# Kernel tuning notes

Hardware: AMD Instinct MI355X
Metric: run time of the kernel (lower is better)

Reference implementation:

```python
import jax, jax.numpy as jnp
import numpy as np

H = 4096   # hidden_size
B = 8      # batch_size
N = 200    # total_nodes (<=200 so the undocumented sampler branch is not taken)
E = 400    # total_edges
TOPK_STARTS = 3   # min(3, nodes_in_batch)
# With max_hops=min(4,2)=2 and max_paths=min(8,4)=4, BFS yields only length-2
# paths and each start contributes paths[:4//3]=1 path: its first valid edge.


def _lin_init(k, fan_in, shape):
    s = 1.0 / np.sqrt(fan_in)
    return jax.random.uniform(k, shape, jnp.float32, -s, s)


def setup_inputs() -> dict:
    key = jax.random.key(0)
    ks = jax.random.split(key, 12)
    return {
        "query": jax.random.normal(ks[0], (B, H), jnp.float32),
        "node_features": jax.random.normal(ks[1], (N, H), jnp.float32),
        "Wq": _lin_init(ks[2], H, (H, H)), "bq": _lin_init(ks[3], H, (H,)),
        "Wn": _lin_init(ks[4], H, (H, H)), "bn": _lin_init(ks[5], H, (H,)),
        "W1": _lin_init(ks[6], H, (H, H)), "b1": _lin_init(ks[7], H, (H,)),
        "W2": _lin_init(ks[8], H, (H, H)), "b2": _lin_init(ks[9], H, (H,)),
        "ln_g": jnp.ones((H,), jnp.float32), "ln_b": jnp.zeros((H,), jnp.float32),
        "edge_index": jax.random.randint(ks[10], (2, E), 0, N),
        "batch_indices": jnp.sort(jax.random.randint(ks[11], (N,), 0, B)),
    }


def reference(query, node_features, Wq, bq, Wn, bn, W1, b1, W2, b2, ln_g, ln_b,
              edge_index, batch_indices):
    qp = query @ Wq.T + bq              # [B,H] query_projection
    npj = node_features @ Wn.T + bn     # [N,H] node_projection

    # cosine similarity (torch F.cosine_similarity, eps=1e-8), masked per batch
    qn = jnp.linalg.norm(qp, axis=-1, keepdims=True)   # [B,1]
    nn_ = jnp.linalg.norm(npj, axis=-1)                # [N]
    sim = (qp @ npj.T) / jnp.maximum(qn * nn_[None, :], 1e-8)   # [B,N]
    node_mask = batch_indices[None, :] == jnp.arange(B)[:, None]  # [B,N]
    sim_m = jnp.where(node_mask, sim, -jnp.inf)
    _, starts = jax.lax.top_k(sim_m, TOPK_STARTS)      # [B,3] global node ids

    # first outgoing edge of each start whose dst lies in the same batch
    src, dst = edge_index[0], edge_index[1]            # [E]
    dst_batch = batch_indices[dst]                     # [E]
    valid = (src[None, None, :] == starts[:, :, None]) & \
            (dst_batch[None, None, :] == jnp.arange(B)[:, None, None])  # [B,3,E]
    order = jnp.where(valid, jnp.arange(E)[None, None, :], E)
    first = jnp.min(order, axis=-1)                    # [B,3]
    has = first < E                                    # [B,3] start has a path
    dst_sel = dst[jnp.minimum(first, E - 1)]           # [B,3]

    # each path = [start, dst]; padded/truncated to max_hops=2 then averaged
    path_feat = 0.5 * (node_features[starts] + node_features[dst_sel])  # [B,3,H]
    cnt = jnp.sum(has, axis=1)                         # [B]
    agg = jnp.sum(path_feat * has[..., None], axis=1) / \
          jnp.maximum(cnt, 1).astype(path_feat.dtype)[:, None]
    h = jax.nn.relu(agg @ W1.T + b1) @ W2.T + b2       # path_aggregator MLP

    # fallback when no paths: mean of projected nodes in the batch
    cntn = jnp.sum(node_mask, axis=1)
    fallback = (node_mask.astype(npj.dtype) @ npj) / \
               jnp.maximum(cntn, 1).astype(npj.dtype)[:, None]
    pr = jnp.where((cnt > 0)[:, None], h, fallback)    # [B,H]

    # dropout is identity in eval mode; LayerNorm(eps=1e-5)
    mu = pr.mean(-1, keepdims=True)
    var = ((pr - mu) ** 2).mean(-1, keepdims=True)
    return (pr - mu) / jnp.sqrt(var + 1e-5) * ln_g + ln_b
```

## Files before the change

kernel.cpp:

```cpp
#include <hip/hip_runtime.h>
#include <math.h>

#define H    4096
#define BB   8
#define NN   200
#define NPAD 208
#define EE   400

typedef __bf16 bf16x8 __attribute__((ext_vector_type(8)));
typedef float f32x4 __attribute__((ext_vector_type(4)));

#define OFF_NFHI  0u
#define OFF_NFLO  (OFF_NFHI + (unsigned)NPAD*H*2u)
#define OFF_QP    (OFF_NFLO + (unsigned)NPAD*H*2u)
#define OFF_NPJ   (OFF_QP   + (unsigned)BB*H*4u)
#define OFF_AGG   (OFF_NPJ  + (unsigned)NN*H*4u)
#define OFF_FALLB (OFF_AGG  + (unsigned)BB*H*4u)
#define OFF_T     (OFF_FALLB+ (unsigned)BB*H*4u)
#define OFF_HB    (OFF_T    + (unsigned)BB*H*4u)
#define OFF_KEY   (OFF_HB   + (unsigned)BB*H*4u)
#define OFF_META  (OFF_KEY  + (unsigned)BB*NN*4u)
#define OFF_LIST  (OFF_META + (unsigned)BB*16*4u)
#define OFF_NPJP  (OFF_LIST + (unsigned)BB*NN*4u)

__device__ __forceinline__ unsigned short f2bf(float x) {
  unsigned int u = __float_as_uint(x);
  u = (u + 0x7fffu + ((u >> 16) & 1u)) >> 16;
  return (unsigned short)u;
}
__device__ __forceinline__ float bf2f(unsigned short b) {
  return __uint_as_float(((unsigned int)b) << 16);
}
__device__ __forceinline__ bf16x8 ld_bf8(const unsigned short* p) {
  union { uint4 u; bf16x8 v; } x;
  x.u = *(const uint4*)p;
  return x.v;
}

__global__ __launch_bounds__(256) void k_split_nf(const float* __restrict__ nf,
                                                  unsigned short* __restrict__ hi,
                                                  unsigned short* __restrict__ lo) {
  int i = blockIdx.x * 256 + threadIdx.x;
  int row = i >> 10;
  int c4 = (i & 1023) * 4;
  float4 v = make_float4(0.f, 0.f, 0.f, 0.f);
  if (row < NN) v = *(const float4*)&nf[(size_t)row * H + c4];
  float xs[4] = {v.x, v.y, v.z, v.w};
  ushort4 hv, lv;
  unsigned short* hp = &hv.x;
  unsigned short* lp = &lv.x;
#pragma unroll
  for (int j = 0; j < 4; j++) {
    unsigned short h = f2bf(xs[j]);
    hp[j] = h;
    lp[j] = f2bf(xs[j] - bf2f(h));
  }
  *(ushort4*)&hi[(size_t)row * H + c4] = hv;
  *(ushort4*)&lo[(size_t)row * H + c4] = lv;
}

__global__ __launch_bounds__(256) void k_gemm_m8(const float* __restrict__ X,
                                                 const float* __restrict__ W,
                                                 const float* __restrict__ bias,
                                                 float* __restrict__ Y, int relu) {
  const int wave = (blockIdx.x * 256 + threadIdx.x) >> 6;
  const int lane = threadIdx.x & 63;
  const int h0 = wave * 2;
  float acc0[8] = {0, 0, 0, 0, 0, 0, 0, 0};
  float acc1[8] = {0, 0, 0, 0, 0, 0, 0, 0};
  const float4* Wr0 = (const float4*)(W + (size_t)h0 * H);
  const float4* Wr1 = (const float4*)(W + (size_t)(h0 + 1) * H);
  const float4* Xv = (const float4*)X;
#pragma unroll 4
  for (int j = 0; j < 16; j++) {
    const int kq = lane + j * 64;
    float4 w0 = Wr0[kq];
    float4 w1 = Wr1[kq];
#pragma unroll
    for (int m = 0; m < 8; m++) {
      float4 x = Xv[m * (H / 4) + kq];
      acc0[m] = fmaf(w0.x, x.x, acc0[m]);
      acc0[m] = fmaf(w0.y, x.y, acc0[m]);
      acc0[m] = fmaf(w0.z, x.z, acc0[m]);
      acc0[m] = fmaf(w0.w, x.w, acc0[m]);
      acc1[m] = fmaf(w1.x, x.x, acc1[m]);
      acc1[m] = fmaf(w1.y, x.y, acc1[m]);
      acc1[m] = fmaf(w1.z, x.z, acc1[m]);
      acc1[m] = fmaf(w1.w, x.w, acc1[m]);
    }
  }
#pragma unroll
  for (int m = 0; m < 8; m++) {
    float a0 = acc0[m], a1 = acc1[m];
#pragma unroll
    for (int off = 32; off > 0; off >>= 1) {
      a0 += __shfl_xor(a0, off, 64);
      a1 += __shfl_xor(a1, off, 64);
    }
    if (lane == 0) {
      float y0 = a0 + bias[h0];
      float y1 = a1 + bias[h0 + 1];
      if (relu) { y0 = fmaxf(y0, 0.f); y1 = fmaxf(y1, 0.f); }
      Y[(size_t)m * H + h0] = y0;
      Y[(size_t)m * H + h0 + 1] = y1;
    }
  }
}

__global__ __launch_bounds__(512, 4) void k_npj_mfma(const unsigned short* __restrict__ nfhi,
                                                     const unsigned short* __restrict__ nflo,
                                                     const float* __restrict__ Wn,
                                                     float* __restrict__ npjp, int nchunks) {
  __shared__ __align__(16) unsigned short Ahi[NPAD * 72];
  __shared__ __align__(16) unsigned short Alo[NPAD * 72];
  __shared__ __align__(16) unsigned short Bhi[64 * 72];
  __shared__ __align__(16) unsigned short Blo[64 * 72];
  const int hblk = blockIdx.x & 63;
  const int kblk = blockIdx.x >> 6;
  const int h0 = hblk * 64;
  const int kbase = kblk * (nchunks * 64);
  const int tid = threadIdx.x;
  const int wid = tid >> 6, lane = tid & 63;
  const int hseg = wid & 1, nseg = wid >> 1;
  const int lrow = lane & 15, lk8 = (lane >> 4) * 8;

  f32x4 acc[4][2];
#pragma unroll
  for (int t = 0; t < 4; t++)
#pragma unroll
    for (int ht = 0; ht < 2; ht++) {
      f32x4 z = {0.f, 0.f, 0.f, 0.f};
      acc[t][ht] = z;
    }

  for (int ck = 0; ck < nchunks; ck++) {
    const int k0 = kbase + ck * 64;
    __syncthreads();
#pragma unroll
    for (int i = 0; i < 4; i++) {
      int idx = tid + i * 512;
      if (idx < (NPAD * 64 / 8)) {
        int row = idx >> 3, c8 = (idx & 7) * 8;
        *(uint4*)&Ahi[row * 72 + c8] = *(const uint4*)&nfhi[(size_t)row * H + k0 + c8];
        *(uint4*)&Alo[row * 72 + c8] = *(const uint4*)&nflo[(size_t)row * H + k0 + c8];
      }
    }
#pragma unroll
    for (int i = 0; i < 2; i++) {
      int idx = tid + i * 512;
      if (idx < 1024) {
        int row = idx >> 4, c4 = (idx & 15) * 4;
        float4 w = *(const float4*)&Wn[(size_t)(h0 + row) * H + k0 + c4];
        float xs[4] = {w.x, w.y, w.z, w.w};
        ushort4 hv, lv;
        unsigned short* hp = &hv.x;
        unsigned short* lp = &lv.x;
#pragma unroll
        for (int j = 0; j < 4; j++) {
          unsigned short hb = f2bf(xs[j]);
          hp[j] = hb;
          lp[j] = f2bf(xs[j] - bf2f(hb));
        }
        *(ushort4*)&Bhi[row * 72 + c4] = hv;
        *(ushort4*)&Blo[row * 72 + c4] = lv;
      }
    }
    __syncthreads();
#pragma unroll
    for (int kf = 0; kf < 2; kf++) {
      const int ko = kf * 32 + lk8;
      bf16x8 bh[2], bl[2];
#pragma unroll
      for (int ht = 0; ht < 2; ht++) {
        int hcol = hseg * 32 + ht * 16 + lrow;
        bh[ht] = ld_bf8(&Bhi[hcol * 72 + ko]);
        bl[ht] = ld_bf8(&Blo[hcol * 72 + ko]);
      }
#pragma unroll
      for (int t = 0; t < 4; t++) {
        if (t == 3 && nseg < 3) continue;
        int tile = nseg * 3 + t;
        int nrow = tile * 16 + lrow;
        bf16x8 ah = ld_bf8(&Ahi[nrow * 72 + ko]);
        bf16x8 al = ld_bf8(&Alo[nrow * 72 + ko]);
#pragma unroll
        for (int ht = 0; ht < 2; ht++) {
          acc[t][ht] = __builtin_amdgcn_mfma_f32_16x16x32_bf16(ah, bh[ht], acc[t][ht], 0, 0, 0);
          acc[t][ht] = __builtin_amdgcn_mfma_f32_16x16x32_bf16(ah, bl[ht], acc[t][ht], 0, 0, 0);
          acc[t][ht] = __builtin_amdgcn_mfma_f32_16x16x32_bf16(al, bh[ht], acc[t][ht], 0, 0, 0);
        }
      }
    }
  }
#pragma unroll
  for (int t = 0; t < 4; t++) {
    if (t == 3 && nseg < 3) continue;
    int tile = nseg * 3 + t;
#pragma unroll
    for (int ht = 0; ht < 2; ht++) {
      int h = h0 + hseg * 32 + ht * 16 + lrow;
#pragma unroll
      for (int r = 0; r < 4; r++) {
        int n = tile * 16 + (lane >> 4) * 4 + r;
        if (n < NN) npjp[((size_t)kblk * NN + n) * H + h] = acc[t][ht][r];
      }
    }
  }
}

__global__ __launch_bounds__(256) void k_npj_reduce(const float* __restrict__ npjp,
                                                    const float* __restrict__ bn,
                                                    float* __restrict__ npj, int ks) {
  int e = blockIdx.x * 256 + threadIdx.x;
  float s = bn[e & (H - 1)];
  for (int kb = 0; kb < ks; kb++) s += npjp[(size_t)kb * NN * H + e];
  npj[e] = s;
}

__global__ __launch_bounds__(256) void k_sim(const float* __restrict__ qp,
                                             const float* __restrict__ npj,
                                             const int* __restrict__ batch,
                                             float* __restrict__ key) {
  const int n = blockIdx.x;
  const int tid = threadIdx.x, lane = tid & 63, wid = tid >> 6;
  __shared__ float red[4 * 9];
  __shared__ float fin[9];
  const float4* pv = (const float4*)(npj + (size_t)n * H);
  const float4* qv = (const float4*)qp;
  float acc[9];
#pragma unroll
  for (int j = 0; j < 9; j++) acc[j] = 0.f;
#pragma unroll
  for (int i = 0; i < 4; i++) {
    float4 p = pv[tid + i * 256];
    acc[0] = fmaf(p.x, p.x, fmaf(p.y, p.y, fmaf(p.z, p.z, fmaf(p.w, p.w, acc[0]))));
#pragma unroll
    for (int b = 0; b < 8; b++) {
      float4 q = qv[b * (H / 4) + tid + i * 256];
      acc[1 + b] = fmaf(p.x, q.x, fmaf(p.y, q.y, fmaf(p.z, q.z, fmaf(p.w, q.w, acc[1 + b]))));
    }
  }
#pragma unroll
  for (int j = 0; j < 9; j++)
#pragma unroll
    for (int off = 32; off > 0; off >>= 1) acc[j] += __shfl_xor(acc[j], off, 64);
  if (lane == 0)
#pragma unroll
    for (int j = 0; j < 9; j++) red[wid * 9 + j] = acc[j];
  __syncthreads();
  if (tid < 9) fin[tid] = red[0 * 9 + tid] + red[1 * 9 + tid] + red[2 * 9 + tid] + red[3 * 9 + tid];
  __syncthreads();
  if (tid < 8) {
    float r = rsqrtf(fmaxf(fin[0], 1e-30f));
    key[tid * NN + n] = (batch[n] == tid) ? fin[1 + tid] * r : -INFINITY;
  }
}

__global__ __launch_bounds__(256) void k_topedges(const float* __restrict__ key,
                                                  const int* __restrict__ edge,
                                                  const int* __restrict__ batch,
                                                  int* __restrict__ meta,
                                                  int* __restrict__ list) {
  const int b = blockIdx.x;
  const int tid = threadIdx.x, lane = tid & 63, wid = tid >> 6;
  __shared__ float key_s[256];
  __shared__ int starts_s[3], firsts_s[3];
  __shared__ float redv[4];
  __shared__ int redi[4];
  key_s[tid] = (tid < NN) ? key[b * NN + tid] : -INFINITY;
  if (tid < 3) firsts_s[tid] = EE;
  __syncthreads();
  for (int s = 0; s < 3; s++) {
    float v = key_s[tid];
    if ((s > 0 && tid == starts_s[0]) || (s > 1 && tid == starts_s[1])) v = -INFINITY;
    int idx = tid;
#pragma unroll
    for (int off = 32; off > 0; off >>= 1) {
      float ov = __shfl_xor(v, off, 64);
      int oi = __shfl_xor(idx, off, 64);
      if (ov > v || (ov == v && oi < idx)) { v = ov; idx = oi; }
    }
    if (lane == 0) { redv[wid] = v; redi[wid] = idx; }
    __syncthreads();
    if (tid == 0) {
      float bv = redv[0]; int bi = redi[0];
#pragma unroll
      for (int w = 1; w < 4; w++)
        if (redv[w] > bv || (redv[w] == bv && redi[w] < bi)) { bv = redv[w]; bi = redi[w]; }
      starts_s[s] = bi;
    }
    __syncthreads();
  }
  for (int e = tid; e < EE; e += 256) {
    int s = edge[e];
    int d = edge[EE + e];
    if (batch[d] == b) {
#pragma unroll
      for (int j = 0; j < 3; j++)
        if (s == starts_s[j]) atomicMin(&firsts_s[j], e);
    }
  }
  if (tid == 64) {
    int c = 0;
    for (int n = 0; n < NN; n++)
      if (batch[n] == b) list[b * NN + c++] = n;
    meta[b * 16 + 10] = c;
  }
  __syncthreads();
  if (tid == 0) {
    int c = 0;
#pragma unroll
    for (int j = 0; j < 3; j++) {
      int f = firsts_s[j];
      meta[b * 16 + j] = starts_s[j];
      meta[b * 16 + 3 + j] = f;
      meta[b * 16 + 6 + j] = edge[EE + (f < EE ? f : EE - 1)];
      c += (f < EE) ? 1 : 0;
    }
    meta[b * 16 + 9] = c;
  }
}

__global__ __launch_bounds__(256) void k_aggfall(const float* __restrict__ nf,
                                                 const float* __restrict__ npj,
                                                 const int* __restrict__ meta,
                                                 const int* __restrict__ list,
                                                 float* __restrict__ agg,
                                                 float* __restrict__ fallb) {
  const int b = blockIdx.y;
  const int col = blockIdx.x * 256 + threadIdx.x;
  const int* m = meta + b * 16;
  const int cnt = m[9], cntn = m[10];
  float a = 0.f;
#pragma unroll
  for (int j = 0; j < 3; j++)
    if (m[3 + j] < EE)
      a += 0.5f * (nf[(size_t)m[j] * H + col] + nf[(size_t)m[6 + j] * H + col]);
  agg[(size_t)b * H + col] = a / (float)(cnt > 0 ? cnt : 1);
  float f = 0.f;
  for (int i = 0; i < cntn; i++) f += npj[(size_t)list[b * NN + i] * H + col];
  fallb[(size_t)b * H + col] = f / (float)(cntn > 0 ? cntn : 1);
}

__global__ __launch_bounds__(256) void k_finalize(const float* __restrict__ hb,
                                                  const float* __restrict__ fallb,
                                                  const int* __restrict__ meta,
                                                  const float* __restrict__ g,
                                                  const float* __restrict__ beta,
                                                  float* __restrict__ out) {
  const int b = blockIdx.x;
  const int tid = threadIdx.x;
  const int wid = tid >> 6, lane = tid & 63;
  __shared__ float red[4];
  const float* src = (meta[b * 16 + 9] > 0) ? &hb[(size_t)b * H] : &fallb[(size_t)b * H];
  float v[16];
  float s = 0.f;
#pragma unroll
  for (int i = 0; i < 16; i++) {
    v[i] = src[tid + i * 256];
    s += v[i];
  }
#pragma unroll
  for (int off = 32; off > 0; off >>= 1) s += __shfl_xor(s, off, 64);
  if (lane == 0) red[wid] = s;
  __syncthreads();
  float mu = (red[0] + red[1] + red[2] + red[3]) * (1.f / H);
  float q = 0.f;
#pragma unroll
  for (int i = 0; i < 16; i++) {
    float d = v[i] - mu;
    q = fmaf(d, d, q);
  }
  __syncthreads();
#pragma unroll
  for (int off = 32; off > 0; off >>= 1) q += __shfl_xor(q, off, 64);
  if (lane == 0) red[wid] = q;
  __syncthreads();
  float var = (red[0] + red[1] + red[2] + red[3]) * (1.f / H);
  float inv = 1.f / sqrtf(var + 1e-5f);
#pragma unroll
  for (int i = 0; i < 16; i++) {
    int col = tid + i * 256;
    out[(size_t)b * H + col] = (v[i] - mu) * inv * g[col] + beta[col];
  }
}

extern "C" void kernel_launch(void* const* d_in, const int* in_sizes, int n_in,
                              void* d_out, int out_size, void* d_ws, size_t ws_size,
                              hipStream_t stream) {
  (void)in_sizes; (void)n_in; (void)out_size;
  const float* query = (const float*)d_in[0];
  const float* nf    = (const float*)d_in[1];
  const float* Wq = (const float*)d_in[2];
  const float* bq = (const float*)d_in[3];
  const float* Wn = (const float*)d_in[4];
  const float* bn = (const float*)d_in[5];
  const float* W1 = (const float*)d_in[6];
  const float* b1 = (const float*)d_in[7];
  const float* W2 = (const float*)d_in[8];
  const float* b2 = (const float*)d_in[9];
  const float* lng = (const float*)d_in[10];
  const float* lnb = (const float*)d_in[11];
  const int* edge  = (const int*)d_in[12];
  const int* batch = (const int*)d_in[13];

  char* ws = (char*)d_ws;
  unsigned short* nfhi = (unsigned short*)(ws + OFF_NFHI);
  unsigned short* nflo = (unsigned short*)(ws + OFF_NFLO);
  float* qp    = (float*)(ws + OFF_QP);
  float* npj   = (float*)(ws + OFF_NPJ);
  float* agg   = (float*)(ws + OFF_AGG);
  float* fallb = (float*)(ws + OFF_FALLB);
  float* tbuf  = (float*)(ws + OFF_T);
  float* hbuf  = (float*)(ws + OFF_HB);
  float* keyb  = (float*)(ws + OFF_KEY);
  int*   meta  = (int*)(ws + OFF_META);
  int*   list  = (int*)(ws + OFF_LIST);
  float* npjp  = (float*)(ws + OFF_NPJP);

  size_t per = (size_t)NN * H * 4u;
  int ks = 1;
  if (ws_size >= (size_t)OFF_NPJP + 8 * per) ks = 8;
  else if (ws_size >= (size_t)OFF_NPJP + 4 * per) ks = 4;
  else if (ws_size >= (size_t)OFF_NPJP + 2 * per) ks = 2;
  int nchunks = 64 / ks;

  k_split_nf<<<dim3(NPAD * (H / 4) / 256), dim3(256), 0, stream>>>(nf, nfhi, nflo);
  k_gemm_m8<<<dim3(512), dim3(256), 0, stream>>>(query, Wq, bq, qp, 0);
  k_npj_mfma<<<dim3(64 * ks), dim3(512), 0, stream>>>(nfhi, nflo, Wn, npjp, nchunks);
  k_npj_reduce<<<dim3(NN * H / 256), dim3(256), 0, stream>>>(npjp, bn, npj, ks);
  k_sim<<<dim3(NN), dim3(256), 0, stream>>>(qp, npj, batch, keyb);
  k_topedges<<<dim3(BB), dim3(256), 0, stream>>>(keyb, edge, batch, meta, list);
  k_aggfall<<<dim3(16, BB), dim3(256), 0, stream>>>(nf, npj, meta, list, agg, fallb);
  k_gemm_m8<<<dim3(512), dim3(256), 0, stream>>>(agg, W1, b1, tbuf, 1);
  k_gemm_m8<<<dim3(512), dim3(256), 0, stream>>>(tbuf, W2, b2, hbuf, 0);
  k_finalize<<<dim3(BB), dim3(256), 0, stream>>>(hbuf, fallb, meta, lng, lnb, (float*)d_out);
}
```

Measured before the change: 367.2 us.

## Move all four GEMMs to split-bf16 32x32 MFMA with pre-packed fragment layouts

The three M=8 FP32 FMA GEMMs (Wq, W1, W2) are replaced by a split-K 32x32x16 bf16 MFMA kernel. It uses hi/lo error compensation, and a combine kernel sums the partials and adds bias and ReLU. The node projection drops its LDS-tiled 16x16 MFMA kernel and uses the same register-only kernel, with node features pre-packed into MFMA fragment order and up to 16-way split-K. Activations for the next GEMM are written directly in packed hi/lo form. The change targets FP32 FMA throughput and LDS staging overhead, at the cost of more launches, partial-sum traffic and in-loop conversion of the weights to bf16.

```diff
diff --git a/kernel.cpp b/kernel.cpp
--- a/kernel.cpp
+++ b/kernel.cpp
@@ -4,24 +4,30 @@
 #define H    4096
 #define BB   8
 #define NN   200
-#define NPAD 208
 #define EE   400
+#define NT_NF 7
+#define KT16 256
+#define HT32 128
+#define KSM8 32
 
 typedef __bf16 bf16x8 __attribute__((ext_vector_type(8)));
-typedef float f32x4 __attribute__((ext_vector_type(4)));
-
-#define OFF_NFHI  0u
-#define OFF_NFLO  (OFF_NFHI + (unsigned)NPAD*H*2u)
-#define OFF_QP    (OFF_NFLO + (unsigned)NPAD*H*2u)
-#define OFF_NPJ   (OFF_QP   + (unsigned)BB*H*4u)
-#define OFF_AGG   (OFF_NPJ  + (unsigned)NN*H*4u)
-#define OFF_FALLB (OFF_AGG  + (unsigned)BB*H*4u)
-#define OFF_T     (OFF_FALLB+ (unsigned)BB*H*4u)
-#define OFF_HB    (OFF_T    + (unsigned)BB*H*4u)
-#define OFF_KEY   (OFF_HB   + (unsigned)BB*H*4u)
-#define OFF_META  (OFF_KEY  + (unsigned)BB*NN*4u)
-#define OFF_LIST  (OFF_META + (unsigned)BB*16*4u)
-#define OFF_NPJP  (OFF_LIST + (unsigned)BB*NN*4u)
+typedef float f32x16 __attribute__((ext_vector_type(16)));
+
+#define OFF_QH   0u
+#define OFF_QL   262144u
+#define OFF_AH   524288u
+#define OFF_AL   786432u
+#define OFF_TH   1048576u
+#define OFF_TL   1310720u
+#define OFF_NFH  1572864u
+#define OFF_NFL  3407872u
+#define OFF_QP   5242880u
+#define OFF_HB   5373952u
+#define OFF_FB   5505024u
+#define OFF_KEY  5636096u
+#define OFF_META 5642496u
+#define OFF_LIST 5643008u
+#define OFF_SH   5650432u
 
 __device__ __forceinline__ unsigned short f2bf(float x) {
   unsigned int u = __float_as_uint(x);
@@ -31,179 +37,143 @@
 __device__ __forceinline__ float bf2f(unsigned short b) {
   return __uint_as_float(((unsigned int)b) << 16);
 }
-__device__ __forceinline__ bf16x8 ld_bf8(const unsigned short* p) {
-  union { uint4 u; bf16x8 v; } x;
-  x.u = *(const uint4*)p;
-  return x.v;
-}
-
-__global__ __launch_bounds__(256) void k_split_nf(const float* __restrict__ nf,
-                                                  unsigned short* __restrict__ hi,
-                                                  unsigned short* __restrict__ lo) {
-  int i = blockIdx.x * 256 + threadIdx.x;
-  int row = i >> 10;
-  int c4 = (i & 1023) * 4;
-  float4 v = make_float4(0.f, 0.f, 0.f, 0.f);
-  if (row < NN) v = *(const float4*)&nf[(size_t)row * H + c4];
-  float xs[4] = {v.x, v.y, v.z, v.w};
-  ushort4 hv, lv;
-  unsigned short* hp = &hv.x;
-  unsigned short* lp = &lv.x;
-#pragma unroll
-  for (int j = 0; j < 4; j++) {
+
+union U8 { unsigned short s[8]; bf16x8 v; uint4 q; };
+
+__global__ __launch_bounds__(256) void k_pack8(const float* __restrict__ X,
+                                               unsigned short* __restrict__ hi,
+                                               unsigned short* __restrict__ lo) {
+  int t = blockIdx.x * 256 + threadIdx.x;
+  int ktile = t >> 6, lane = t & 63;
+  int row = lane & 31;
+  int k = ktile * 16 + (lane >> 5) * 8;
+  float4 a = make_float4(0.f, 0.f, 0.f, 0.f), b = a;
+  if (row < 8) {
+    a = *(const float4*)&X[(size_t)row * H + k];
+    b = *(const float4*)&X[(size_t)row * H + k + 4];
+  }
+  float xs[8] = {a.x, a.y, a.z, a.w, b.x, b.y, b.z, b.w};
+  U8 hv, lv;
+#pragma unroll
+  for (int j = 0; j < 8; j++) {
     unsigned short h = f2bf(xs[j]);
-    hp[j] = h;
-    lp[j] = f2bf(xs[j] - bf2f(h));
-  }
-  *(ushort4*)&hi[(size_t)row * H + c4] = hv;
-  *(ushort4*)&lo[(size_t)row * H + c4] = lv;
-}
-
-__global__ __launch_bounds__(256) void k_gemm_m8(const float* __restrict__ X,
-                                                 const float* __restrict__ W,
-                                                 const float* __restrict__ bias,
-                                                 float* __restrict__ Y, int relu) {
-  const int wave = (blockIdx.x * 256 + threadIdx.x) >> 6;
+    hv.s[j] = h;
+    lv.s[j] = f2bf(xs[j] - bf2f(h));
+  }
+  *(uint4*)&hi[(size_t)t * 8] = hv.q;
+  *(uint4*)&lo[(size_t)t * 8] = lv.q;
+}
+
+__global__ __launch_bounds__(256) void k_pack_nf(const float* __restrict__ nf,
+                                                 unsigned short* __restrict__ hi,
+                                                 unsigned short* __restrict__ lo) {
+  int t = blockIdx.x * 256 + threadIdx.x;
+  int ktile = t / (NT_NF * 64);
+  int rem = t - ktile * (NT_NF * 64);
+  int ntile = rem >> 6, lane = rem & 63;
+  int n = ntile * 32 + (lane & 31);
+  int k = ktile * 16 + (lane >> 5) * 8;
+  float4 a = make_float4(0.f, 0.f, 0.f, 0.f), b = a;
+  if (n < NN) {
+    a = *(const float4*)&nf[(size_t)n * H + k];
+    b = *(const float4*)&nf[(size_t)n * H + k + 4];
+  }
+  float xs[8] = {a.x, a.y, a.z, a.w, b.x, b.y, b.z, b.w};
+  U8 hv, lv;
+#pragma unroll
+  for (int j = 0; j < 8; j++) {
+    unsigned short h = f2bf(xs[j]);
+    hv.s[j] = h;
+    lv.s[j] = f2bf(xs[j] - bf2f(h));
+  }
+  *(uint4*)&hi[(size_t)t * 8] = hv.q;
+  *(uint4*)&lo[(size_t)t * 8] = lv.q;
+}
+
+template<int NT, int MINW>
+__global__ __launch_bounds__(256, MINW) void k_mfma32(const unsigned short* __restrict__ ahi,
+                                                      const unsigned short* __restrict__ alo,
+                                                      const float* __restrict__ W,
+                                                      float* __restrict__ partial,
+                                                      int nk, int nrows) {
+  const int gw = (blockIdx.x * 256 + threadIdx.x) >> 6;
   const int lane = threadIdx.x & 63;
-  const int h0 = wave * 2;
-  float acc0[8] = {0, 0, 0, 0, 0, 0, 0, 0};
-  float acc1[8] = {0, 0, 0, 0, 0, 0, 0, 0};
-  const float4* Wr0 = (const float4*)(W + (size_t)h0 * H);
-  const float4* Wr1 = (const float4*)(W + (size_t)(h0 + 1) * H);
-  const float4* Xv = (const float4*)X;
-#pragma unroll 4
-  for (int j = 0; j < 16; j++) {
-    const int kq = lane + j * 64;
-    float4 w0 = Wr0[kq];
-    float4 w1 = Wr1[kq];
-#pragma unroll
-    for (int m = 0; m < 8; m++) {
-      float4 x = Xv[m * (H / 4) + kq];
-      acc0[m] = fmaf(w0.x, x.x, acc0[m]);
-      acc0[m] = fmaf(w0.y, x.y, acc0[m]);
-      acc0[m] = fmaf(w0.z, x.z, acc0[m]);
-      acc0[m] = fmaf(w0.w, x.w, acc0[m]);
-      acc1[m] = fmaf(w1.x, x.x, acc1[m]);
-      acc1[m] = fmaf(w1.y, x.y, acc1[m]);
-      acc1[m] = fmaf(w1.z, x.z, acc1[m]);
-      acc1[m] = fmaf(w1.w, x.w, acc1[m]);
-    }
-  }
-#pragma unroll
-  for (int m = 0; m < 8; m++) {
-    float a0 = acc0[m], a1 = acc1[m];
-#pragma unroll
-    for (int off = 32; off > 0; off >>= 1) {
-      a0 += __shfl_xor(a0, off, 64);
-      a1 += __shfl_xor(a1, off, 64);
-    }
-    if (lane == 0) {
-      float y0 = a0 + bias[h0];
-      float y1 = a1 + bias[h0 + 1];
-      if (relu) { y0 = fmaxf(y0, 0.f); y1 = fmaxf(y1, 0.f); }
-      Y[(size_t)m * H + h0] = y0;
-      Y[(size_t)m * H + h0 + 1] = y1;
-    }
-  }
-}
-
-__global__ __launch_bounds__(512, 4) void k_npj_mfma(const unsigned short* __restrict__ nfhi,
-                                                     const unsigned short* __restrict__ nflo,
-                                                     const float* __restrict__ Wn,
-                                                     float* __restrict__ npjp, int nchunks) {
-  __shared__ __align__(16) unsigned short Ahi[NPAD * 72];
-  __shared__ __align__(16) unsigned short Alo[NPAD * 72];
-  __shared__ __align__(16) unsigned short Bhi[64 * 72];
-  __shared__ __align__(16) unsigned short Blo[64 * 72];
-  const int hblk = blockIdx.x & 63;
-  const int kblk = blockIdx.x >> 6;
-  const int h0 = hblk * 64;
-  const int kbase = kblk * (nchunks * 64);
-  const int tid = threadIdx.x;
-  const int wid = tid >> 6, lane = tid & 63;
-  const int hseg = wid & 1, nseg = wid >> 1;
-  const int lrow = lane & 15, lk8 = (lane >> 4) * 8;
-
-  f32x4 acc[4][2];
-#pragma unroll
-  for (int t = 0; t < 4; t++)
-#pragma unroll
-    for (int ht = 0; ht < 2; ht++) {
-      f32x4 z = {0.f, 0.f, 0.f, 0.f};
-      acc[t][ht] = z;
-    }
-
-  for (int ck = 0; ck < nchunks; ck++) {
-    const int k0 = kbase + ck * 64;
-    __syncthreads();
-#pragma unroll
-    for (int i = 0; i < 4; i++) {
-      int idx = tid + i * 512;
-      if (idx < (NPAD * 64 / 8)) {
-        int row = idx >> 3, c8 = (idx & 7) * 8;
-        *(uint4*)&Ahi[row * 72 + c8] = *(const uint4*)&nfhi[(size_t)row * H + k0 + c8];
-        *(uint4*)&Alo[row * 72 + c8] = *(const uint4*)&nflo[(size_t)row * H + k0 + c8];
-      }
-    }
-#pragma unroll
-    for (int i = 0; i < 2; i++) {
-      int idx = tid + i * 512;
-      if (idx < 1024) {
-        int row = idx >> 4, c4 = (idx & 15) * 4;
-        float4 w = *(const float4*)&Wn[(size_t)(h0 + row) * H + k0 + c4];
-        float xs[4] = {w.x, w.y, w.z, w.w};
-        ushort4 hv, lv;
-        unsigned short* hp = &hv.x;
-        unsigned short* lp = &lv.x;
-#pragma unroll
-        for (int j = 0; j < 4; j++) {
-          unsigned short hb = f2bf(xs[j]);
-          hp[j] = hb;
-          lp[j] = f2bf(xs[j] - bf2f(hb));
-        }
-        *(ushort4*)&Bhi[row * 72 + c4] = hv;
-        *(ushort4*)&Blo[row * 72 + c4] = lv;
-      }
-    }
-    __syncthreads();
-#pragma unroll
-    for (int kf = 0; kf < 2; kf++) {
-      const int ko = kf * 32 + lk8;
-      bf16x8 bh[2], bl[2];
-#pragma unroll
-      for (int ht = 0; ht < 2; ht++) {
-        int hcol = hseg * 32 + ht * 16 + lrow;
-        bh[ht] = ld_bf8(&Bhi[hcol * 72 + ko]);
-        bl[ht] = ld_bf8(&Blo[hcol * 72 + ko]);
-      }
-#pragma unroll
-      for (int t = 0; t < 4; t++) {
-        if (t == 3 && nseg < 3) continue;
-        int tile = nseg * 3 + t;
-        int nrow = tile * 16 + lrow;
-        bf16x8 ah = ld_bf8(&Ahi[nrow * 72 + ko]);
-        bf16x8 al = ld_bf8(&Alo[nrow * 72 + ko]);
-#pragma unroll
-        for (int ht = 0; ht < 2; ht++) {
-          acc[t][ht] = __builtin_amdgcn_mfma_f32_16x16x32_bf16(ah, bh[ht], acc[t][ht], 0, 0, 0);
-          acc[t][ht] = __builtin_amdgcn_mfma_f32_16x16x32_bf16(ah, bl[ht], acc[t][ht], 0, 0, 0);
-          acc[t][ht] = __builtin_amdgcn_mfma_f32_16x16x32_bf16(al, bh[ht], acc[t][ht], 0, 0, 0);
-        }
-      }
-    }
-  }
-#pragma unroll
-  for (int t = 0; t < 4; t++) {
-    if (t == 3 && nseg < 3) continue;
-    int tile = nseg * 3 + t;
-#pragma unroll
-    for (int ht = 0; ht < 2; ht++) {
-      int h = h0 + hseg * 32 + ht * 16 + lrow;
-#pragma unroll
-      for (int r = 0; r < 4; r++) {
-        int n = tile * 16 + (lane >> 4) * 4 + r;
-        if (n < NN) npjp[((size_t)kblk * NN + n) * H + h] = acc[t][ht][r];
-      }
+  const int htile = gw & (HT32 - 1);
+  const int kb = gw >> 7;
+  const int h0 = htile * 32;
+  const int ktile0 = kb * nk;
+  const int l31 = lane & 31, lg = lane >> 5;
+
+  f32x16 acc[NT];
+#pragma unroll
+  for (int nt = 0; nt < NT; nt++)
+#pragma unroll
+    for (int i = 0; i < 16; i++) acc[nt][i] = 0.f;
+
+  const float* wbase = W + (size_t)(h0 + l31) * H + lg * 8;
+
+#pragma unroll 2
+  for (int ck = 0; ck < nk; ++ck) {
+    const int ktile = ktile0 + ck;
+    const float4* wp = (const float4*)(wbase + ktile * 16);
+    float4 w0 = wp[0], w1 = wp[1];
+    float xs[8] = {w0.x, w0.y, w0.z, w0.w, w1.x, w1.y, w1.z, w1.w};
+    U8 bh, bl;
+#pragma unroll
+    for (int j = 0; j < 8; j++) {
+      unsigned short hb = f2bf(xs[j]);
+      bh.s[j] = hb;
+      bl.s[j] = f2bf(xs[j] - bf2f(hb));
+    }
+#pragma unroll
+    for (int nt = 0; nt < NT; nt++) {
+      U8 ah, al;
+      ah.q = *(const uint4*)&ahi[((size_t)(ktile * NT + nt) * 64 + lane) * 8];
+      al.q = *(const uint4*)&alo[((size_t)(ktile * NT + nt) * 64 + lane) * 8];
+      acc[nt] = __builtin_amdgcn_mfma_f32_32x32x16_bf16(ah.v, bh.v, acc[nt], 0, 0, 0);
+      acc[nt] = __builtin_amdgcn_mfma_f32_32x32x16_bf16(ah.v, bl.v, acc[nt], 0, 0, 0);
+      acc[nt] = __builtin_amdgcn_mfma_f32_32x32x16_bf16(al.v, bh.v, acc[nt], 0, 0, 0);
+    }
+  }
+#pragma unroll
+  for (int nt = 0; nt < NT; nt++)
+#pragma unroll
+    for (int r = 0; r < 16; r++) {
+      int n = nt * 32 + (r & 3) + 8 * (r >> 2) + 4 * lg;
+      if (n < nrows)
+        partial[((size_t)kb * nrows + n) * H + h0 + l31] = acc[nt][r];
+    }
+}
+
+__global__ __launch_bounds__(256) void k_combine8(const float* __restrict__ partial,
+                                                  const float* __restrict__ bias,
+                                                  float* __restrict__ Y,
+                                                  unsigned short* __restrict__ phi,
+                                                  unsigned short* __restrict__ plo,
+                                                  int relu) {
+  int t = blockIdx.x * 256 + threadIdx.x;
+  int row = t >> 10, c4 = (t & 1023) * 4;
+  float4 s = *(const float4*)&bias[c4];
+#pragma unroll
+  for (int kb = 0; kb < KSM8; kb++) {
+    float4 p = *(const float4*)&partial[((size_t)kb * 8 + row) * H + c4];
+    s.x += p.x; s.y += p.y; s.z += p.z; s.w += p.w;
+  }
+  if (relu) {
+    s.x = fmaxf(s.x, 0.f); s.y = fmaxf(s.y, 0.f);
+    s.z = fmaxf(s.z, 0.f); s.w = fmaxf(s.w, 0.f);
+  }
+  if (Y) *(float4*)&Y[(size_t)row * H + c4] = s;
+  if (phi) {
+    float xs[4] = {s.x, s.y, s.z, s.w};
+#pragma unroll
+    for (int j = 0; j < 4; j++) {
+      int k = c4 + j;
+      int lane = row + ((k >> 3) & 1) * 32;
+      size_t idx = ((size_t)(k >> 4) * 64 + lane) * 8 + (k & 7);
+      unsigned short hb = f2bf(xs[j]);
+      phi[idx] = hb;
+      plo[idx] = f2bf(xs[j] - bf2f(hb));
     }
   }
 }
@@ -211,10 +181,14 @@
 __global__ __launch_bounds__(256) void k_npj_reduce(const float* __restrict__ npjp,
                                                     const float* __restrict__ bn,
                                                     float* __restrict__ npj, int ks) {
-  int e = blockIdx.x * 256 + threadIdx.x;
-  float s = bn[e & (H - 1)];
-  for (int kb = 0; kb < ks; kb++) s += npjp[(size_t)kb * NN * H + e];
-  npj[e] = s;
+  int e4 = blockIdx.x * 256 + threadIdx.x;
+  int c4 = e4 & 1023;
+  float4 s = ((const float4*)bn)[c4];
+  for (int kb = 0; kb < ks; kb++) {
+    float4 p = ((const float4*)npjp)[(size_t)kb * (NN * H / 4) + e4];
+    s.x += p.x; s.y += p.y; s.z += p.z; s.w += p.w;
+  }
+  ((float4*)npj)[e4] = s;
 }
 
 __global__ __launch_bounds__(256) void k_sim(const float* __restrict__ qp,
@@ -325,7 +299,8 @@
                                                  const float* __restrict__ npj,
                                                  const int* __restrict__ meta,
                                                  const int* __restrict__ list,
-                                                 float* __restrict__ agg,
+                                                 unsigned short* __restrict__ ahi,
+                                                 unsigned short* __restrict__ alo,
                                                  float* __restrict__ fallb) {
   const int b = blockIdx.y;
   const int col = blockIdx.x * 256 + threadIdx.x;
@@ -336,7 +311,14 @@
   for (int j = 0; j < 3; j++)
     if (m[3 + j] < EE)
       a += 0.5f * (nf[(size_t)m[j] * H + col] + nf[(size_t)m[6 + j] * H + col]);
-  agg[(size_t)b * H + col] = a / (float)(cnt > 0 ? cnt : 1);
+  a /= (float)(cnt > 0 ? cnt : 1);
+  {
+    int lane = b + ((col >> 3) & 1) * 32;
+    size_t idx = ((size_t)(col >> 4) * 64 + lane) * 8 + (col & 7);
+    unsigned short hb = f2bf(a);
+    ahi[idx] = hb;
+    alo[idx] = f2bf(a - bf2f(hb));
+  }
   float f = 0.f;
   for (int i = 0; i < cntn; i++) f += npj[(size_t)list[b * NN + i] * H + col];
   fallb[(size_t)b * H + col] = f / (float)(cntn > 0 ? cntn : 1);
@@ -405,34 +387,44 @@
   const int* batch = (const int*)d_in[13];
 
   char* ws = (char*)d_ws;
-  unsigned short* nfhi = (unsigned short*)(ws + OFF_NFHI);
-  unsigned short* nflo = (unsigned short*)(ws + OFF_NFLO);
+  unsigned short* qh  = (unsigned short*)(ws + OFF_QH);
+  unsigned short* ql  = (unsigned short*)(ws + OFF_QL);
+  unsigned short* ah  = (unsigned short*)(ws + OFF_AH);
+  unsigned short* al  = (unsigned short*)(ws + OFF_AL);
+  unsigned short* th  = (unsigned short*)(ws + OFF_TH);
+  unsigned short* tl  = (unsigned short*)(ws + OFF_TL);
+  unsigned short* nfh = (unsigned short*)(ws + OFF_NFH);
+  unsigned short* nfl = (unsigned short*)(ws + OFF_NFL);
   float* qp    = (float*)(ws + OFF_QP);
-  float* npj   = (float*)(ws + OFF_NPJ);
-  float* agg   = (float*)(ws + OFF_AGG);
-  float* fallb = (float*)(ws + OFF_FALLB);
-  float* tbuf  = (float*)(ws + OFF_T);
   float* hbuf  = (float*)(ws + OFF_HB);
+  float* fallb = (float*)(ws + OFF_FB);
   float* keyb  = (float*)(ws + OFF_KEY);
   int*   meta  = (int*)(ws + OFF_META);
   int*   list  = (int*)(ws + OFF_LIST);
-  float* npjp  = (float*)(ws + OFF_NPJP);
+  float* p8    = (float*)(ws + OFF_SH);
+  float* npjp  = (float*)(ws + OFF_SH);
 
   size_t per = (size_t)NN * H * 4u;
-  int ks = 1;
-  if (ws_size >= (size_t)OFF_NPJP + 8 * per) ks = 8;
-  else if (ws_size >= (size_t)OFF_NPJP + 4 * per) ks = 4;
-  else if (ws_size >= (size_t)OFF_NPJP + 2 * per) ks = 2;
-  int nchunks = 64 / ks;
-
-  k_split_nf<<<dim3(NPAD * (H / 4) / 256), dim3(256), 0, stream>>>(nf, nfhi, nflo);
-  k_gemm_m8<<<dim3(512), dim3(256), 0, stream>>>(query, Wq, bq, qp, 0);
-  k_npj_mfma<<<dim3(64 * ks), dim3(512), 0, stream>>>(nfhi, nflo, Wn, npjp, nchunks);
-  k_npj_reduce<<<dim3(NN * H / 256), dim3(256), 0, stream>>>(npjp, bn, npj, ks);
+  int ks = 4;
+  if (ws_size >= (size_t)OFF_SH + 16 * per + per) ks = 16;
+  else if (ws_size >= (size_t)OFF_SH + 8 * per + per) ks = 8;
+  int nk = KT16 / ks;
+  size_t shmax = (size_t)ks * per;
+  if (shmax < 4194304u) shmax = 4194304u;
+  float* npj = (float*)(ws + OFF_SH + shmax);
+
+  k_pack8<<<dim3(64), dim3(256), 0, stream>>>(query, qh, ql);
+  k_mfma32<1, 4><<<dim3(HT32 * KSM8 / 4), dim3(256), 0, stream>>>(qh, ql, Wq, p8, KT16 / KSM8, 8);
+  k_combine8<<<dim3(32), dim3(256), 0, stream>>>(p8, bq, qp, nullptr, nullptr, 0);
+  k_pack_nf<<<dim3(KT16 * NT_NF * 64 / 256), dim3(256), 0, stream>>>(nf, nfh, nfl);
+  k_mfma32<NT_NF, 2><<<dim3(HT32 * ks / 4), dim3(256), 0, stream>>>(nfh, nfl, Wn, npjp, nk, NN);
+  k_npj_reduce<<<dim3(NN * H / 4 / 256), dim3(256), 0, stream>>>(npjp, bn, npj, ks);
   k_sim<<<dim3(NN), dim3(256), 0, stream>>>(qp, npj, batch, keyb);
   k_topedges<<<dim3(BB), dim3(256), 0, stream>>>(keyb, edge, batch, meta, list);
-  k_aggfall<<<dim3(16, BB), dim3(256), 0, stream>>>(nf, npj, meta, list, agg, fallb);
-  k_gemm_m8<<<dim3(512), dim3(256), 0, stream>>>(agg, W1, b1, tbuf, 1);
-  k_gemm_m8<<<dim3(512), dim3(256), 0, stream>>>(tbuf, W2, b2, hbuf, 0);
+  k_aggfall<<<dim3(16, BB), dim3(256), 0, stream>>>(nf, npj, meta, list, ah, al, fallb);
+  k_mfma32<1, 4><<<dim3(HT32 * KSM8 / 4), dim3(256), 0, stream>>>(ah, al, W1, p8, KT16 / KSM8, 8);
+  k_combine8<<<dim3(32), dim3(256), 0, stream>>>(p8, b1, nullptr, th, tl, 1);
+  k_mfma32<1, 4><<<dim3(HT32 * KSM8 / 4), dim3(256), 0, stream>>>(th, tl, W2, p8, KT16 / KSM8, 8);
+  k_combine8<<<dim3(32), dim3(256), 0, stream>>>(p8, b2, hbuf, nullptr, nullptr, 0);
   k_finalize<<<dim3(BB), dim3(256), 0, stream>>>(hbuf, fallb, meta, lng, lnb, (float*)d_out);
 }
```

After: 405.8 us. 10.5% more time.
